# Kernel tuning notes

Measured on AMD Instinct MI355X. Metric: run time of the kernel, lower is better.

## Reference

```python
import jax, jax.numpy as jnp
import numpy as np

N_NODES = 50000
N_EDGES = 800000
D = 128  # in_dim == hidden_dim


def setup_inputs() -> dict:
    key = jax.random.key(0)
    k1, k2, k3, k4 = jax.random.split(key, 4)
    x = jax.random.normal(k1, (N_NODES, D), dtype=jnp.float32)
    edge_index = jax.random.randint(k2, (2, N_EDGES), 0, N_NODES, dtype=jnp.int64)
    # Glorot-ish scale for square weights
    scale = 1.0 / np.sqrt(D)
    W1 = jax.random.normal(k3, (D, D), dtype=jnp.float32) * scale
    W2 = jax.random.normal(k4, (D, D), dtype=jnp.float32) * scale
    b1 = jnp.zeros((D,), dtype=jnp.float32)
    b2 = jnp.zeros((D,), dtype=jnp.float32)
    return {"x": x, "edge_index": edge_index, "W1": W1, "b1": b1, "W2": W2, "b2": b2}


def _gcn_layer(x, W, b, src, dst, norm, n):
    # PyG GCNConv: h = x @ W, then symmetric-normalized scatter-add, then + bias
    h = x @ W                                   # [N, D] dense GEMM
    msg = h[src] * norm[:, None]                # [E', D] gather + scale
    out = jax.ops.segment_sum(msg, dst, num_segments=n)  # scatter-add
    return out + b


def reference(x, edge_index, W1, b1, W2, b2):
    n = x.shape[0]
    # add self-loops (GCNConv default add_self_loops=True)
    loops = jnp.arange(n, dtype=edge_index.dtype)
    src = jnp.concatenate([edge_index[0], loops])
    dst = jnp.concatenate([edge_index[1], loops])
    # symmetric normalization: deg^{-1/2}[src] * deg^{-1/2}[dst]
    deg = jax.ops.segment_sum(jnp.ones_like(src, dtype=x.dtype), dst, num_segments=n)
    dinv = jax.lax.rsqrt(jnp.maximum(deg, 1.0))  # deg >= 1 due to self-loops
    norm = dinv[src] * dinv[dst]
    # layer 1: conv -> relu (dropout is identity in eval mode)
    h = jax.nn.relu(_gcn_layer(x, W1, b1, src, dst, norm, n))
    # layer 2 (cut='c2'): conv -> relu
    h = jax.nn.relu(_gcn_layer(h, W2, b2, src, dst, norm, n))
    return h
```

## Files before the change

### kernel.cpp

```cpp
#include <hip/hip_runtime.h>

#define NN 50000
#define NE 800000
#define DD 128
#define NSTRIP 3125
#define NB 196
#define CHUNK 4096
#define MAXB 6144

#define OF_BCUR  0
#define OF_DINV  256
#define OF_OFFS2 50432
#define OF_TMP   150528
#define OF_CSRU  1723392
#define OF_G     2509824
#define OF_X2    5709824
#define OF_W1H   12109824
#define OF_W1L   12118016
#define OF_W2H   12126208
#define OF_W2L   12134400

typedef __attribute__((ext_vector_type(8))) short bf8_t;
typedef __attribute__((ext_vector_type(8))) unsigned short us8;
typedef __attribute__((ext_vector_type(4))) float f32x4;

static __device__ __forceinline__ unsigned short f2bf(float f) {
    unsigned int u = __float_as_uint(f);
    unsigned int r = (u + 0x7fffu + ((u >> 16) & 1u)) >> 16;
    return (unsigned short)r;
}
static __device__ __forceinline__ float bf2f(unsigned short h) {
    return __uint_as_float(((unsigned int)h) << 16);
}

__global__ void k_wconv(const float* __restrict__ W1, const float* __restrict__ W2,
                        ushort* __restrict__ w1h, ushort* __restrict__ w1l,
                        ushort* __restrict__ w2h, ushort* __restrict__ w2l,
                        int* __restrict__ bcur) {
    if (blockIdx.x == 0) bcur[threadIdx.x] = 0;
    int gg = blockIdx.x * 256 + threadIdx.x;
    const float* W = (gg < 2048) ? W1 : W2;
    ushort* wh = (gg < 2048) ? w1h : w2h;
    ushort* wl = (gg < 2048) ? w1l : w2l;
    int g = gg & 2047;
    int ntile = g >> 8;
    int kk = (g >> 6) & 3;
    int lane = g & 63;
    int k0 = kk * 32 + ((lane >> 4) * 8);
    int col = ntile * 16 + (lane & 15);
#pragma unroll
    for (int j = 0; j < 8; ++j) {
        float w = W[(k0 + j) * DD + col];
        unsigned short h = f2bf(w);
        wh[(size_t)g * 8 + j] = h;
        wl[(size_t)g * 8 + j] = f2bf(w - bf2f(h));
    }
}

__global__ void k_shuf(const int* __restrict__ src, const int* __restrict__ dst,
                       int* __restrict__ bcur, unsigned int* __restrict__ tmp) {
    __shared__ int lcnt[256];
    __shared__ int lbase[256];
    __shared__ int lcur[256];
    int tid = threadIdx.x;
    lcnt[tid] = 0;
    __syncthreads();
    int e0 = blockIdx.x * CHUNK;
    int e1 = e0 + CHUNK; if (e1 > NE) e1 = NE;
    for (int e = e0 + tid; e < e1; e += 256)
        atomicAdd(&lcnt[dst[e] >> 8], 1);
    __syncthreads();
    if (lcnt[tid]) lbase[tid] = atomicAdd(&bcur[tid], lcnt[tid]);
    lcur[tid] = 0;
    __syncthreads();
    for (int e = e0 + tid; e < e1; e += 256) {
        int d = dst[e], s = src[e];
        int b = d >> 8;
        int r = atomicAdd(&lcur[b], 1);
        tmp[(size_t)b * MAXB + lbase[b] + r] =
            ((unsigned int)s << 8) | (unsigned int)(d & 255);
    }
}

__global__ __launch_bounds__(256) void k_sort(const int* __restrict__ bcur,
                                              const unsigned int* __restrict__ tmp,
                                              ushort* __restrict__ csru,
                                              int2* __restrict__ offs2,
                                              float* __restrict__ dinv) {
    __shared__ unsigned int ent[MAXB];
    __shared__ int cnt[256];
    __shared__ int boff[256];
    __shared__ int cur[256];
    int b = blockIdx.x, tid = threadIdx.x;
    int base = b * MAXB;
    int nb = bcur[b];
    cnt[tid] = 0;
    __syncthreads();
    for (int i = tid; i < nb; i += 256) {
        unsigned int v = tmp[base + i];
        ent[i] = v;
        atomicAdd(&cnt[v & 255], 1);
    }
    __syncthreads();
    int v = cnt[tid];
    boff[tid] = v;
    __syncthreads();
    for (int o = 1; o < 256; o <<= 1) {
        int t = (tid >= o) ? boff[tid - o] : 0;
        __syncthreads();
        boff[tid] += t;
        __syncthreads();
    }
    int excl = boff[tid] - v;
    int node = b * 256 + tid;
    if (node < NN) {
        offs2[node] = make_int2(base + excl, base + excl + v);
        dinv[node] = rsqrtf((float)(v + 1));
    }
    cur[tid] = excl;
    __syncthreads();
    for (int i = tid; i < nb; i += 256) {
        unsigned int e = ent[i];
        int bin = e & 255;
        int r = atomicAdd(&cur[bin], 1);
        csru[base + r] = (ushort)(e >> 8);
    }
}

__global__ __launch_bounds__(256) void k_mgemm(const float* __restrict__ X,
                                               const ushort* __restrict__ wh,
                                               const ushort* __restrict__ wl,
                                               const float* __restrict__ dinv,
                                               ushort* __restrict__ G) {
    int wave = threadIdx.x >> 6;
    int lane = threadIdx.x & 63;
    int strip = blockIdx.x * 4 + wave;
    if (strip >= NSTRIP) return;
    int rb = strip << 4;
    int m = lane & 15;
    int quad = lane >> 4;
    const float* ar = X + (size_t)(rb + m) * DD;
    f32x4 acc[8];
#pragma unroll
    for (int t = 0; t < 8; ++t) acc[t] = (f32x4){0.f, 0.f, 0.f, 0.f};
#pragma unroll
    for (int kk = 0; kk < 4; ++kk) {
        float4 xa = *(const float4*)(ar + kk * 32 + quad * 8);
        float4 xb = *(const float4*)(ar + kk * 32 + quad * 8 + 4);
        float xs[8] = {xa.x, xa.y, xa.z, xa.w, xb.x, xb.y, xb.z, xb.w};
        bf8_t ah, al;
#pragma unroll
        for (int j = 0; j < 8; ++j) {
            unsigned short hh = f2bf(xs[j]);
            ah[j] = (short)hh;
            al[j] = (short)f2bf(xs[j] - bf2f(hh));
        }
#pragma unroll
        for (int t = 0; t < 8; ++t) {
            size_t bo = ((size_t)(t * 4 + kk) * 64 + lane) * 8;
            bf8_t bh = *(const bf8_t*)(wh + bo);
            bf8_t bl = *(const bf8_t*)(wl + bo);
            acc[t] = __builtin_amdgcn_mfma_f32_16x16x32_bf16(ah, bh, acc[t], 0, 0, 0);
            acc[t] = __builtin_amdgcn_mfma_f32_16x16x32_bf16(ah, bl, acc[t], 0, 0, 0);
            acc[t] = __builtin_amdgcn_mfma_f32_16x16x32_bf16(al, bh, acc[t], 0, 0, 0);
        }
    }
    float dv[4];
#pragma unroll
    for (int r = 0; r < 4; ++r) dv[r] = dinv[rb + quad * 4 + r];
#pragma unroll
    for (int t = 0; t < 8; ++t) {
#pragma unroll
        for (int r = 0; r < 4; ++r)
            G[(size_t)(rb + quad * 4 + r) * DD + t * 16 + m] = f2bf(dv[r] * acc[t][r]);
    }
}

__global__ void k_agg(const ushort* __restrict__ g, const float* __restrict__ dinv,
                      const int2* __restrict__ offs2, const ushort* __restrict__ csru,
                      const float* __restrict__ bias, float* __restrict__ outf) {
    int wave = threadIdx.x >> 6;
    int lane = threadIdx.x & 63;
    int node = blockIdx.x * 4 + wave;
    int q = lane >> 4;
    int l = lane & 15;
    float a0[8] = {0.f, 0.f, 0.f, 0.f, 0.f, 0.f, 0.f, 0.f};
    float a1[8] = {0.f, 0.f, 0.f, 0.f, 0.f, 0.f, 0.f, 0.f};
    float a2[8] = {0.f, 0.f, 0.f, 0.f, 0.f, 0.f, 0.f, 0.f};
    float a3[8] = {0.f, 0.f, 0.f, 0.f, 0.f, 0.f, 0.f, 0.f};
    int2 oe = offs2[node];
    int e  = oe.x + q;
    int e1 = oe.y;
    for (; e + 12 < e1; e += 16) {
        int s0 = csru[e];
        int s1 = csru[e + 4];
        int s2 = csru[e + 8];
        int s3 = csru[e + 12];
        us8 v0 = *(const us8*)(g + (size_t)s0 * DD + 8 * l);
        us8 v1 = *(const us8*)(g + (size_t)s1 * DD + 8 * l);
        us8 v2 = *(const us8*)(g + (size_t)s2 * DD + 8 * l);
        us8 v3 = *(const us8*)(g + (size_t)s3 * DD + 8 * l);
#pragma unroll
        for (int j = 0; j < 8; ++j) {
            a0[j] += bf2f(v0[j]);
            a1[j] += bf2f(v1[j]);
            a2[j] += bf2f(v2[j]);
            a3[j] += bf2f(v3[j]);
        }
    }
    for (; e < e1; e += 4) {
        int s0 = csru[e];
        us8 v0 = *(const us8*)(g + (size_t)s0 * DD + 8 * l);
#pragma unroll
        for (int j = 0; j < 8; ++j) a0[j] += bf2f(v0[j]);
    }
    if (q == 0) {
        us8 v = *(const us8*)(g + (size_t)node * DD + 8 * l);
#pragma unroll
        for (int j = 0; j < 8; ++j) a0[j] += bf2f(v[j]);
    }
#pragma unroll
    for (int j = 0; j < 8; ++j) {
        a0[j] += a1[j] + a2[j] + a3[j];
        a0[j] += __shfl_xor(a0[j], 16, 64);
        a0[j] += __shfl_xor(a0[j], 32, 64);
    }
    if (q == 0) {
        float di = dinv[node];
        float* op = outf + (size_t)node * DD + 8 * l;
        const float* bp = bias + 8 * l;
        float4 o0, o1;
        o0.x = fmaxf(di * a0[0] + bp[0], 0.f);
        o0.y = fmaxf(di * a0[1] + bp[1], 0.f);
        o0.z = fmaxf(di * a0[2] + bp[2], 0.f);
        o0.w = fmaxf(di * a0[3] + bp[3], 0.f);
        o1.x = fmaxf(di * a0[4] + bp[4], 0.f);
        o1.y = fmaxf(di * a0[5] + bp[5], 0.f);
        o1.z = fmaxf(di * a0[6] + bp[6], 0.f);
        o1.w = fmaxf(di * a0[7] + bp[7], 0.f);
        *(float4*)op = o0;
        *(float4*)(op + 4) = o1;
    }
}

extern "C" void kernel_launch(void* const* d_in, const int* in_sizes, int n_in,
                              void* d_out, int out_size, void* d_ws, size_t ws_size,
                              hipStream_t stream) {
    const float* x  = (const float*)d_in[0];
    const int*   ei = (const int*)d_in[1];
    const float* W1 = (const float*)d_in[2];
    const float* b1 = (const float*)d_in[3];
    const float* W2 = (const float*)d_in[4];
    const float* b2 = (const float*)d_in[5];
    float* out = (float*)d_out;

    const int* src = ei;
    const int* dst = ei + NE;

    int*          wsi  = (int*)d_ws;
    float*        wsf  = (float*)d_ws;
    ushort*       wsu  = (ushort*)d_ws;
    unsigned int* wsuw = (unsigned int*)d_ws;
    int*    bcur  = wsi + OF_BCUR;
    float*  dinv  = wsf + OF_DINV;
    int2*   offs2 = (int2*)(wsi + OF_OFFS2);
    unsigned int* tmp = wsuw + OF_TMP;
    ushort* csru  = wsu + (size_t)OF_CSRU * 2;
    ushort* gbuf  = wsu + (size_t)OF_G * 2;
    float*  x2    = wsf + OF_X2;
    ushort* w1h   = wsu + (size_t)OF_W1H * 2;
    ushort* w1l   = wsu + (size_t)OF_W1L * 2;
    ushort* w2h   = wsu + (size_t)OF_W2H * 2;
    ushort* w2l   = wsu + (size_t)OF_W2L * 2;

    const int chunks = (NE + CHUNK - 1) / CHUNK;

    hipLaunchKernelGGL(k_wconv, dim3(16), dim3(256), 0, stream,
                       W1, W2, w1h, w1l, w2h, w2l, bcur);
    hipLaunchKernelGGL(k_shuf,  dim3(chunks), dim3(256), 0, stream, src, dst, bcur, tmp);
    hipLaunchKernelGGL(k_sort,  dim3(NB), dim3(256), 0, stream, bcur, tmp, csru, offs2, dinv);

    const int gblocks = (NSTRIP + 3) / 4;

    hipLaunchKernelGGL(k_mgemm, dim3(gblocks), dim3(256), 0, stream, x, w1h, w1l, dinv, gbuf);
    hipLaunchKernelGGL(k_agg,   dim3(NN / 4), dim3(256), 0, stream,
                       gbuf, dinv, offs2, csru, b1, x2);
    hipLaunchKernelGGL(k_mgemm, dim3(gblocks), dim3(256), 0, stream, x2, w2h, w2l, dinv, gbuf);
    hipLaunchKernelGGL(k_agg,   dim3(NN / 4), dim3(256), 0, stream,
                       gbuf, dinv, offs2, csru, b2, out);
}
```

Measured before the change: 219.6 us.

## Fuse layer-1 aggregation with layer-2 GEMM into one kernel

Adds k_aggmm, which aggregates neighbor rows for 16 nodes per block, applies bias and ReLU into shared memory, then runs the split-bf16 MFMA GEMM with W2 and writes the scaled bf16 result directly. This drops one kernel launch and the fp32 round trip of the intermediate hidden matrix (write then re-read). In exchange each block does 4 nodes per wave serially before the GEMM, which may lower gather parallelism and latency hiding compared with the separate aggregation kernel.

Measured after the change: 214.1 us. 1.03x faster.

```diff
diff --git a/kernel.cpp b/kernel.cpp
--- a/kernel.cpp
+++ b/kernel.cpp
@@ -13,12 +13,12 @@
 #define OF_OFFS2 50432
 #define OF_TMP   150528
 #define OF_CSRU  1723392
-#define OF_G     2509824
-#define OF_X2    5709824
-#define OF_W1H   12109824
-#define OF_W1L   12118016
-#define OF_W2H   12126208
-#define OF_W2L   12134400
+#define OF_G1    2509824
+#define OF_G2    5709824
+#define OF_W1H   8909824
+#define OF_W1L   8918016
+#define OF_W2H   8926208
+#define OF_W2L   8934400
 
 typedef __attribute__((ext_vector_type(8))) short bf8_t;
 typedef __attribute__((ext_vector_type(8))) unsigned short us8;
@@ -173,6 +173,114 @@
 #pragma unroll
         for (int r = 0; r < 4; ++r)
             G[(size_t)(rb + quad * 4 + r) * DD + t * 16 + m] = f2bf(dv[r] * acc[t][r]);
+    }
+}
+
+__global__ __launch_bounds__(256) void k_aggmm(const ushort* __restrict__ g1,
+                                               const float* __restrict__ dinv,
+                                               const int2* __restrict__ offs2,
+                                               const ushort* __restrict__ csru,
+                                               const float* __restrict__ b1,
+                                               const ushort* __restrict__ w2h,
+                                               const ushort* __restrict__ w2l,
+                                               ushort* __restrict__ g2) {
+    __shared__ float xs[16][132];
+    int wave = threadIdx.x >> 6;
+    int lane = threadIdx.x & 63;
+    int rb = blockIdx.x * 16;
+    int q = lane >> 4;
+    int l = lane & 15;
+    const float* bp = b1 + 8 * l;
+    for (int nn = 0; nn < 4; ++nn) {
+        int node = rb + wave * 4 + nn;
+        float a0[8] = {0.f, 0.f, 0.f, 0.f, 0.f, 0.f, 0.f, 0.f};
+        float a1[8] = {0.f, 0.f, 0.f, 0.f, 0.f, 0.f, 0.f, 0.f};
+        float a2[8] = {0.f, 0.f, 0.f, 0.f, 0.f, 0.f, 0.f, 0.f};
+        float a3[8] = {0.f, 0.f, 0.f, 0.f, 0.f, 0.f, 0.f, 0.f};
+        int2 oe = offs2[node];
+        int e  = oe.x + q;
+        int e1 = oe.y;
+        for (; e + 12 < e1; e += 16) {
+            int s0 = csru[e];
+            int s1 = csru[e + 4];
+            int s2 = csru[e + 8];
+            int s3 = csru[e + 12];
+            us8 v0 = *(const us8*)(g1 + (size_t)s0 * DD + 8 * l);
+            us8 v1 = *(const us8*)(g1 + (size_t)s1 * DD + 8 * l);
+            us8 v2 = *(const us8*)(g1 + (size_t)s2 * DD + 8 * l);
+            us8 v3 = *(const us8*)(g1 + (size_t)s3 * DD + 8 * l);
+#pragma unroll
+            for (int j = 0; j < 8; ++j) {
+                a0[j] += bf2f(v0[j]);
+                a1[j] += bf2f(v1[j]);
+                a2[j] += bf2f(v2[j]);
+                a3[j] += bf2f(v3[j]);
+            }
+        }
+        for (; e < e1; e += 4) {
+            int s0 = csru[e];
+            us8 v0 = *(const us8*)(g1 + (size_t)s0 * DD + 8 * l);
+#pragma unroll
+            for (int j = 0; j < 8; ++j) a0[j] += bf2f(v0[j]);
+        }
+        if (q == 0) {
+            us8 v = *(const us8*)(g1 + (size_t)node * DD + 8 * l);
+#pragma unroll
+            for (int j = 0; j < 8; ++j) a0[j] += bf2f(v[j]);
+        }
+#pragma unroll
+        for (int j = 0; j < 8; ++j) {
+            a0[j] += a1[j] + a2[j] + a3[j];
+            a0[j] += __shfl_xor(a0[j], 16, 64);
+            a0[j] += __shfl_xor(a0[j], 32, 64);
+        }
+        if (q == 0) {
+            float di = dinv[node];
+            float* xr = &xs[wave * 4 + nn][8 * l];
+#pragma unroll
+            for (int j = 0; j < 8; ++j)
+                xr[j] = fmaxf(di * a0[j] + bp[j], 0.f);
+        }
+    }
+    __syncthreads();
+    int m = lane & 15;
+    int quad = lane >> 4;
+    f32x4 acc[2];
+    acc[0] = (f32x4){0.f, 0.f, 0.f, 0.f};
+    acc[1] = (f32x4){0.f, 0.f, 0.f, 0.f};
+#pragma unroll
+    for (int kk = 0; kk < 4; ++kk) {
+        const float* xr = &xs[m][kk * 32 + quad * 8];
+        float4 xa = *(const float4*)xr;
+        float4 xb = *(const float4*)(xr + 4);
+        float xv[8] = {xa.x, xa.y, xa.z, xa.w, xb.x, xb.y, xb.z, xb.w};
+        bf8_t ah, al;
+#pragma unroll
+        for (int j = 0; j < 8; ++j) {
+            unsigned short hh = f2bf(xv[j]);
+            ah[j] = (short)hh;
+            al[j] = (short)f2bf(xv[j] - bf2f(hh));
+        }
+#pragma unroll
+        for (int tt = 0; tt < 2; ++tt) {
+            int t = wave * 2 + tt;
+            size_t bo = ((size_t)(t * 4 + kk) * 64 + lane) * 8;
+            bf8_t bh = *(const bf8_t*)(w2h + bo);
+            bf8_t bl = *(const bf8_t*)(w2l + bo);
+            acc[tt] = __builtin_amdgcn_mfma_f32_16x16x32_bf16(ah, bh, acc[tt], 0, 0, 0);
+            acc[tt] = __builtin_amdgcn_mfma_f32_16x16x32_bf16(ah, bl, acc[tt], 0, 0, 0);
+            acc[tt] = __builtin_amdgcn_mfma_f32_16x16x32_bf16(al, bh, acc[tt], 0, 0, 0);
+        }
+    }
+    float dv[4];
+#pragma unroll
+    for (int r = 0; r < 4; ++r) dv[r] = dinv[rb + quad * 4 + r];
+#pragma unroll
+    for (int tt = 0; tt < 2; ++tt) {
+        int t = wave * 2 + tt;
+#pragma unroll
+        for (int r = 0; r < 4; ++r)
+            g2[(size_t)(rb + quad * 4 + r) * DD + t * 16 + m] = f2bf(dv[r] * acc[tt][r]);
     }
 }
 
@@ -266,8 +374,8 @@
     int2*   offs2 = (int2*)(wsi + OF_OFFS2);
     unsigned int* tmp = wsuw + OF_TMP;
     ushort* csru  = wsu + (size_t)OF_CSRU * 2;
-    ushort* gbuf  = wsu + (size_t)OF_G * 2;
-    float*  x2    = wsf + OF_X2;
+    ushort* g1    = wsu + (size_t)OF_G1 * 2;
+    ushort* g2    = wsu + (size_t)OF_G2 * 2;
     ushort* w1h   = wsu + (size_t)OF_W1H * 2;
     ushort* w1l   = wsu + (size_t)OF_W1L * 2;
     ushort* w2h   = wsu + (size_t)OF_W2H * 2;
@@ -282,10 +390,9 @@
 
     const int gblocks = (NSTRIP + 3) / 4;
 
-    hipLaunchKernelGGL(k_mgemm, dim3(gblocks), dim3(256), 0, stream, x, w1h, w1l, dinv, gbuf);
+    hipLaunchKernelGGL(k_mgemm, dim3(gblocks), dim3(256), 0, stream, x, w1h, w1l, dinv, g1);
+    hipLaunchKernelGGL(k_aggmm, dim3(NSTRIP), dim3(256), 0, stream,
+                       g1, dinv, offs2, csru, b1, w2h, w2l, g2);
     hipLaunchKernelGGL(k_agg,   dim3(NN / 4), dim3(256), 0, stream,
-                       gbuf, dinv, offs2, csru, b1, x2);
-    hipLaunchKernelGGL(k_mgemm, dim3(gblocks), dim3(256), 0, stream, x2, w2h, w2l, dinv, gbuf);
-    hipLaunchKernelGGL(k_agg,   dim3(NN / 4), dim3(256), 0, stream,
-                       gbuf, dinv, offs2, csru, b2, out);
-}
+                       g2, dinv, offs2, csru, b2, out);
+}
```
